# Kernel tuning notes

Measured on AMD Instinct MI355X. Metric: run time of the kernel, lower is better.

The kernel has to match this reference:

```python
import jax, jax.numpy as jnp
import numpy as np

S, B, C, H, W = 2, 100, 5, 224, 224


def setup_inputs() -> dict:
    key = jax.random.key(0)
    ks = jax.random.split(key, 10)
    patches = jax.random.uniform(ks[0], (S, B, C, H, W), jnp.float32)
    translation = jax.random.uniform(ks[1], (S, B, 2), jnp.float32, -0.8, 0.8)
    rotation = jax.random.uniform(ks[2], (S, B), jnp.float32, -np.pi, np.pi)
    scale = jax.random.uniform(ks[3], (S, B), jnp.float32, 0.7, 1.3)
    squeeze = jax.random.uniform(ks[4], (S, B), jnp.float32, 0.8, 1.2)
    shear = jax.random.uniform(ks[5], (S, B), jnp.float32, -0.2, 0.2)
    reds = jax.random.uniform(ks[6], (S, B), jnp.float32, 0.1, 0.5)
    greens = jax.random.uniform(ks[7], (S, B), jnp.float32, 0.1, 0.5)
    blues = jax.random.uniform(ks[8], (S, B), jnp.float32, 0.1, 0.5)
    orders = jax.random.uniform(ks[9], (S, B), jnp.float32)
    return dict(patches=patches, translation=translation, rotation=rotation,
                scale=scale, squeeze=squeeze, shear=shear,
                reds=reds, greens=greens, blues=blues, orders=orders)


def _forward(patches, translation, rotation, scale, squeeze, shear,
             reds, greens, blues, orders):
    s_, b_, c_, h_, w_ = patches.shape
    z = jnp.zeros_like(rotation)
    o = jnp.ones_like(rotation)

    def m3(a11, a12, a13, a21, a22, a23):
        # [S,B,3,3] affine matrix from per-(pop,patch) scalar entries
        r1 = jnp.stack([a11, a12, a13], -1)
        r2 = jnp.stack([a21, a22, a23], -1)
        r3 = jnp.stack([z, z, o], -1)
        return jnp.stack([r1, r2, r3], -2)

    cs, sn = jnp.cos(rotation), jnp.sin(rotation)
    # scale @ rotation @ shear @ translation (same order as the torch module)
    M = (m3(scale * squeeze, z, z, z, scale, z)
         @ m3(cs, -sn, z, sn, cs, z)
         @ m3(o, shear, z, z, o, z)
         @ m3(o, z, translation[..., 0], z, o, translation[..., 1]))
    theta = M[..., :2, :].reshape(s_ * b_, 2, 3)

    # F.affine_grid with align_corners=True: normalized coords in [-1,1]
    xs = jnp.linspace(-1.0, 1.0, w_)[None, :]   # varies along width
    ys = jnp.linspace(-1.0, 1.0, h_)[:, None]   # varies along height
    gx = theta[:, 0, 0, None, None] * xs + theta[:, 0, 1, None, None] * ys + theta[:, 0, 2, None, None]
    gy = theta[:, 1, 0, None, None] * xs + theta[:, 1, 1, None, None] * ys + theta[:, 1, 2, None, None]

    # F.grid_sample bilinear, align_corners=True, zero padding
    ix = (gx + 1.0) * 0.5 * (w_ - 1)
    iy = (gy + 1.0) * 0.5 * (h_ - 1)
    ix0 = jnp.floor(ix)
    iy0 = jnp.floor(iy)
    wx = ix - ix0
    wy = iy - iy0
    ix0i = ix0.astype(jnp.int32)
    iy0i = iy0.astype(jnp.int32)

    P = patches.reshape(s_ * b_, c_, h_, w_)
    gather = jax.vmap(lambda img, y, x: img[:, y, x])  # [C,H,W] per image

    def corner(dy, dx):
        yy = iy0i + dy
        xx = ix0i + dx
        valid = ((yy >= 0) & (yy < h_) & (xx >= 0) & (xx < w_)).astype(patches.dtype)
        v = gather(P, jnp.clip(yy, 0, h_ - 1), jnp.clip(xx, 0, w_ - 1))
        wgt = (wx if dx == 1 else 1.0 - wx) * (wy if dy == 1 else 1.0 - wy) * valid
        return v * wgt[:, None]

    warped = corner(0, 0) + corner(0, 1) + corner(1, 0) + corner(1, 1)
    warped = warped.reshape(s_, b_, c_, h_, w_)

    # RGB colour transform: multiply channels by [r, g, b, 1, order]
    colours = jnp.stack([reds, greens, blues, jnp.ones_like(reds), orders], axis=2)[..., None, None]
    x = warped * colours

    # transparency render: premultiply RGB by alpha, sum over patches, clamp
    rgb = x[:, :, :3] * x[:, :, 3:4]
    y = jnp.clip(rgb.sum(axis=1), 0.0, 1.0)
    return jnp.transpose(y, (0, 2, 3, 1))  # [S,H,W,3]


def reference(patches, translation, rotation, scale, squeeze, shear,
              reds, greens, blues, orders):
    return _forward(patches, translation, rotation, scale, squeeze, shear,
                    reds, greens, blues, orders)
```

## Files before the change

kernel.cpp:

```cpp
#include <hip/hip_runtime.h>

#define SS 2
#define BB 100
#define CC 5
#define HH 224
#define WW 224
#define HW (HH * WW)
#define OUTN (SS * HW * 3)
#define BCHUNK 20
#define NCHUNK (BB / BCHUNK)
#define TILE 16
#define TPD (WW / TILE)
#define TILES_PER_S (TPD * TPD)

__global__ __launch_bounds__(256) void k_reduce(const float* __restrict__ ws,
                                                float* __restrict__ out, int n) {
    int i = blockIdx.x * blockDim.x + threadIdx.x;
    if (i < n) {
        float v = 0.0f;
        #pragma unroll
        for (int c = 0; c < NCHUNK; ++c) v += ws[(size_t)c * OUTN + i];
        out[i] = fminf(fmaxf(v, 0.0f), 1.0f);
    }
}

__global__ __launch_bounds__(256) void k_zero(float* __restrict__ out, int n) {
    int i = blockIdx.x * blockDim.x + threadIdx.x;
    if (i < n) out[i] = 0.0f;
}
__global__ __launch_bounds__(256) void k_clamp(float* __restrict__ out, int n) {
    int i = blockIdx.x * blockDim.x + threadIdx.x;
    if (i < n) { float v = out[i]; out[i] = fminf(fmaxf(v, 0.0f), 1.0f); }
}

template <bool MODE_WS>
__global__ __launch_bounds__(256) void k_main(
    const float* __restrict__ patches,
    const float* __restrict__ tr, const float* __restrict__ rot,
    const float* __restrict__ sc, const float* __restrict__ sq,
    const float* __restrict__ sh, const float* __restrict__ re,
    const float* __restrict__ gr, const float* __restrict__ bl,
    float* __restrict__ dst)
{
    __shared__ float tb[BCHUNK][9];

    const int rem   = blockIdx.x % (SS * TILES_PER_S);
    const int chunk = blockIdx.x / (SS * TILES_PER_S);
    const int s     = rem / TILES_PER_S;
    const int tile  = rem % TILES_PER_S;
    const int tileY = tile / TPD;
    const int tileX = tile % TPD;

    const int tx = threadIdx.x & (TILE - 1);
    const int ty = threadIdx.x >> 4;
    const int w  = tileX * TILE + tx;
    const int h  = tileY * TILE + ty;

    if (threadIdx.x < BCHUNK) {
        const int b = chunk * BCHUNK + threadIdx.x;
        const int i = s * BB + b;
        const float a  = sc[i] * sq[i];
        const float s2 = sc[i];
        float sn, cn;
        sincosf(rot[i], &sn, &cn);
        const float shv = sh[i];
        const float tx_ = tr[2 * i], ty_ = tr[2 * i + 1];
        const float t00 = a * cn;
        const float t01 = a * (cn * shv - sn);
        const float t10 = s2 * sn;
        const float t11 = s2 * (sn * shv + cn);
        tb[threadIdx.x][0] = t00;
        tb[threadIdx.x][1] = t01;
        tb[threadIdx.x][2] = t00 * tx_ + t01 * ty_;
        tb[threadIdx.x][3] = t10;
        tb[threadIdx.x][4] = t11;
        tb[threadIdx.x][5] = t10 * tx_ + t11 * ty_;
        tb[threadIdx.x][6] = re[i];
        tb[threadIdx.x][7] = gr[i];
        tb[threadIdx.x][8] = bl[i];
    }
    __syncthreads();

    const float xs = -1.0f + 2.0f * (float)w / (float)(WW - 1);
    const float ys = -1.0f + 2.0f * (float)h / (float)(HH - 1);

    float accR = 0.0f, accG = 0.0f, accB = 0.0f;

    const float* Pbase = patches + (size_t)s * BB * CC * HW
                                 + (size_t)chunk * BCHUNK * CC * HW;

    for (int bb = 0; bb < BCHUNK; ++bb) {
        const float gx = tb[bb][0] * xs + tb[bb][1] * ys + tb[bb][2];
        const float gy = tb[bb][3] * xs + tb[bb][4] * ys + tb[bb][5];
        const float ix = (gx + 1.0f) * 0.5f * (float)(WW - 1);
        const float iy = (gy + 1.0f) * 0.5f * (float)(HH - 1);

        if (ix <= -1.0f || ix >= (float)WW || iy <= -1.0f || iy >= (float)HH) continue;

        const float ix0f = floorf(ix), iy0f = floorf(iy);
        const float wx = ix - ix0f, wy = iy - iy0f;
        const int ix0 = (int)ix0f, iy0 = (int)iy0f;

        const int x0 = max(ix0, 0);
        const int x1 = min(ix0 + 1, WW - 1);
        const int y0 = max(iy0, 0);
        const int y1 = min(iy0 + 1, HH - 1);

        const float vx0 = (ix0 >= 0)     ? 1.0f : 0.0f;
        const float vx1 = (ix0 + 1 < WW) ? 1.0f : 0.0f;
        const float vy0 = (iy0 >= 0)     ? 1.0f : 0.0f;
        const float vy1 = (iy0 + 1 < HH) ? 1.0f : 0.0f;

        const float w00 = (1.0f - wx) * (1.0f - wy) * vx0 * vy0;
        const float w01 = wx * (1.0f - wy) * vx1 * vy0;
        const float w10 = (1.0f - wx) * wy * vx0 * vy1;
        const float w11 = wx * wy * vx1 * vy1;

        const int i00 = y0 * WW + x0;
        const int i01 = y0 * WW + x1;
        const int i10 = y1 * WW + x0;
        const int i11 = y1 * WW + x1;

        const float* Pb = Pbase + (size_t)bb * CC * HW;

        float chv[4];
        #pragma unroll
        for (int c = 0; c < 4; ++c) {
            const float* Pc = Pb + (size_t)c * HW;
            chv[c] = Pc[i00] * w00 + Pc[i01] * w01 + Pc[i10] * w10 + Pc[i11] * w11;
        }
        const float alpha = chv[3];
        accR += chv[0] * tb[bb][6] * alpha;
        accG += chv[1] * tb[bb][7] * alpha;
        accB += chv[2] * tb[bb][8] * alpha;
    }

    const int pix = s * HW + h * WW + w;
    const size_t o = (size_t)pix * 3;
    if (MODE_WS) {
        float* p = dst + (size_t)chunk * OUTN + o;
        p[0] = accR; p[1] = accG; p[2] = accB;
    } else {
        atomicAdd(&dst[o + 0], accR);
        atomicAdd(&dst[o + 1], accG);
        atomicAdd(&dst[o + 2], accB);
    }
}

extern "C" void kernel_launch(void* const* d_in, const int* in_sizes, int n_in,
                              void* d_out, int out_size, void* d_ws, size_t ws_size,
                              hipStream_t stream) {
    const float* patches = (const float*)d_in[0];
    const float* tr      = (const float*)d_in[1];
    const float* rot     = (const float*)d_in[2];
    const float* sc      = (const float*)d_in[3];
    const float* sq      = (const float*)d_in[4];
    const float* sh      = (const float*)d_in[5];
    const float* re      = (const float*)d_in[6];
    const float* gr      = (const float*)d_in[7];
    const float* bl      = (const float*)d_in[8];
    float* out = (float*)d_out;

    const int nblkOut = (out_size + 255) / 256;
    const int grid    = SS * TILES_PER_S * NCHUNK;

    if (ws_size >= (size_t)NCHUNK * OUTN * sizeof(float)) {
        float* ws = (float*)d_ws;
        k_main<true><<<grid, 256, 0, stream>>>(patches, tr, rot, sc, sq, sh, re, gr, bl, ws);
        k_reduce<<<nblkOut, 256, 0, stream>>>(ws, out, out_size);
    } else {
        k_zero<<<nblkOut, 256, 0, stream>>>(out, out_size);
        k_main<false><<<grid, 256, 0, stream>>>(patches, tr, rot, sc, sq, sh, re, gr, bl, out);
        k_clamp<<<nblkOut, 256, 0, stream>>>(out, out_size);
    }
}
```

Measured before the change: 361.7 us.

## Repack patches into interleaved RGBA float4 layout before bilinear sampling

Adds a pre-pass that transposes the planar RGB+alpha channels of every patch into an interleaved float4 buffer in workspace, so each bilinear corner fetch becomes one 16-byte load instead of four scattered scalar loads. The chunk size per block is halved, doubling the grid and the partial-sum buffer reduced at the end. In exchange it adds a full read and write of about 160 MB of patch data per call, and it only runs if the workspace is large enough.

```diff
diff --git a/kernel.cpp b/kernel.cpp
--- a/kernel.cpp
+++ b/kernel.cpp
@@ -6,12 +6,30 @@
 #define HH 224
 #define WW 224
 #define HW (HH * WW)
+#define IMGN (SS * BB)
 #define OUTN (SS * HW * 3)
-#define BCHUNK 20
+#define BCHUNK 10
 #define NCHUNK (BB / BCHUNK)
 #define TILE 16
 #define TPD (WW / TILE)
 #define TILES_PER_S (TPD * TPD)
+
+#define RGBA_FLOATS ((size_t)IMGN * HW * 4)
+#define PART_FLOATS ((size_t)NCHUNK * OUTN)
+
+__global__ __launch_bounds__(256) void k_repack(const float* __restrict__ patches,
+                                                float4* __restrict__ rgba) {
+    const int i = blockIdx.x * 256 + threadIdx.x;
+    const int img = i / HW;
+    const int hw  = i - img * HW;
+    const float* base = patches + (size_t)img * CC * HW + hw;
+    float4 v;
+    v.x = base[0];
+    v.y = base[HW];
+    v.z = base[2 * HW];
+    v.w = base[3 * HW];
+    rgba[i] = v;
+}
 
 __global__ __launch_bounds__(256) void k_reduce(const float* __restrict__ ws,
                                                 float* __restrict__ out, int n) {
@@ -33,29 +51,9 @@
     if (i < n) { float v = out[i]; out[i] = fminf(fmaxf(v, 0.0f), 1.0f); }
 }
 
-template <bool MODE_WS>
-__global__ __launch_bounds__(256) void k_main(
-    const float* __restrict__ patches,
-    const float* __restrict__ tr, const float* __restrict__ rot,
-    const float* __restrict__ sc, const float* __restrict__ sq,
-    const float* __restrict__ sh, const float* __restrict__ re,
-    const float* __restrict__ gr, const float* __restrict__ bl,
-    float* __restrict__ dst)
-{
-    __shared__ float tb[BCHUNK][9];
-
-    const int rem   = blockIdx.x % (SS * TILES_PER_S);
-    const int chunk = blockIdx.x / (SS * TILES_PER_S);
-    const int s     = rem / TILES_PER_S;
-    const int tile  = rem % TILES_PER_S;
-    const int tileY = tile / TPD;
-    const int tileX = tile % TPD;
-
-    const int tx = threadIdx.x & (TILE - 1);
-    const int ty = threadIdx.x >> 4;
-    const int w  = tileX * TILE + tx;
-    const int h  = tileY * TILE + ty;
-
+__device__ __forceinline__ void setup_tb(float (*tb)[9], int s, int chunk,
+    const float* tr, const float* rot, const float* sc, const float* sq,
+    const float* sh, const float* re, const float* gr, const float* bl) {
     if (threadIdx.x < BCHUNK) {
         const int b = chunk * BCHUNK + threadIdx.x;
         const int i = s * BB + b;
@@ -79,6 +77,112 @@
         tb[threadIdx.x][7] = gr[i];
         tb[threadIdx.x][8] = bl[i];
     }
+}
+
+__global__ __launch_bounds__(256) void k_main_rgba(
+    const float4* __restrict__ rgba,
+    const float* __restrict__ tr, const float* __restrict__ rot,
+    const float* __restrict__ sc, const float* __restrict__ sq,
+    const float* __restrict__ sh, const float* __restrict__ re,
+    const float* __restrict__ gr, const float* __restrict__ bl,
+    float* __restrict__ dst)
+{
+    __shared__ float tb[BCHUNK][9];
+
+    const int rem   = blockIdx.x % (SS * TILES_PER_S);
+    const int chunk = blockIdx.x / (SS * TILES_PER_S);
+    const int s     = rem / TILES_PER_S;
+    const int tile  = rem % TILES_PER_S;
+    const int tileY = tile / TPD;
+    const int tileX = tile % TPD;
+
+    const int tx = threadIdx.x & (TILE - 1);
+    const int ty = threadIdx.x >> 4;
+    const int w  = tileX * TILE + tx;
+    const int h  = tileY * TILE + ty;
+
+    setup_tb(tb, s, chunk, tr, rot, sc, sq, sh, re, gr, bl);
+    __syncthreads();
+
+    const float xs = -1.0f + 2.0f * (float)w / (float)(WW - 1);
+    const float ys = -1.0f + 2.0f * (float)h / (float)(HH - 1);
+
+    float accR = 0.0f, accG = 0.0f, accB = 0.0f;
+
+    const float4* Ibase = rgba + (size_t)(s * BB + chunk * BCHUNK) * HW;
+
+    for (int bb = 0; bb < BCHUNK; ++bb) {
+        const float gx = tb[bb][0] * xs + tb[bb][1] * ys + tb[bb][2];
+        const float gy = tb[bb][3] * xs + tb[bb][4] * ys + tb[bb][5];
+        const float ix = (gx + 1.0f) * 0.5f * (float)(WW - 1);
+        const float iy = (gy + 1.0f) * 0.5f * (float)(HH - 1);
+
+        if (ix <= -1.0f || ix >= (float)WW || iy <= -1.0f || iy >= (float)HH) continue;
+
+        const float ix0f = floorf(ix), iy0f = floorf(iy);
+        const float wx = ix - ix0f, wy = iy - iy0f;
+        const int ix0 = (int)ix0f, iy0 = (int)iy0f;
+
+        const int x0 = max(ix0, 0);
+        const int x1 = min(ix0 + 1, WW - 1);
+        const int y0 = max(iy0, 0);
+        const int y1 = min(iy0 + 1, HH - 1);
+
+        const float vx0 = (ix0 >= 0)     ? 1.0f : 0.0f;
+        const float vx1 = (ix0 + 1 < WW) ? 1.0f : 0.0f;
+        const float vy0 = (iy0 >= 0)     ? 1.0f : 0.0f;
+        const float vy1 = (iy0 + 1 < HH) ? 1.0f : 0.0f;
+
+        const float w00 = (1.0f - wx) * (1.0f - wy) * vx0 * vy0;
+        const float w01 = wx * (1.0f - wy) * vx1 * vy0;
+        const float w10 = (1.0f - wx) * wy * vx0 * vy1;
+        const float w11 = wx * wy * vx1 * vy1;
+
+        const float4* Ib = Ibase + (size_t)bb * HW;
+        const float4 v00 = Ib[y0 * WW + x0];
+        const float4 v01 = Ib[y0 * WW + x1];
+        const float4 v10 = Ib[y1 * WW + x0];
+        const float4 v11 = Ib[y1 * WW + x1];
+
+        const float cr = fmaf(v00.x, w00, fmaf(v01.x, w01, fmaf(v10.x, w10, v11.x * w11)));
+        const float cg = fmaf(v00.y, w00, fmaf(v01.y, w01, fmaf(v10.y, w10, v11.y * w11)));
+        const float cb = fmaf(v00.z, w00, fmaf(v01.z, w01, fmaf(v10.z, w10, v11.z * w11)));
+        const float ca = fmaf(v00.w, w00, fmaf(v01.w, w01, fmaf(v10.w, w10, v11.w * w11)));
+
+        accR = fmaf(cr * tb[bb][6], ca, accR);
+        accG = fmaf(cg * tb[bb][7], ca, accG);
+        accB = fmaf(cb * tb[bb][8], ca, accB);
+    }
+
+    const int pix = s * HW + h * WW + w;
+    float* p = dst + (size_t)chunk * OUTN + (size_t)pix * 3;
+    p[0] = accR; p[1] = accG; p[2] = accB;
+}
+
+template <bool MODE_WS>
+__global__ __launch_bounds__(256) void k_main_planar(
+    const float* __restrict__ patches,
+    const float* __restrict__ tr, const float* __restrict__ rot,
+    const float* __restrict__ sc, const float* __restrict__ sq,
+    const float* __restrict__ sh, const float* __restrict__ re,
+    const float* __restrict__ gr, const float* __restrict__ bl,
+    float* __restrict__ dst)
+{
+    __shared__ float tb[BCHUNK][9];
+
+    const int rem   = blockIdx.x % (SS * TILES_PER_S);
+    const int chunk = blockIdx.x / (SS * TILES_PER_S);
+    const int s     = rem / TILES_PER_S;
+    const int tile  = rem % TILES_PER_S;
+    const int tileY = tile / TPD;
+    const int tileX = tile % TPD;
+
+    const int tx = threadIdx.x & (TILE - 1);
+    const int ty = threadIdx.x >> 4;
+    const int w  = tileX * TILE + tx;
+    const int h  = tileY * TILE + ty;
+
+    setup_tb(tb, s, chunk, tr, rot, sc, sq, sh, re, gr, bl);
     __syncthreads();
 
     const float xs = -1.0f + 2.0f * (float)w / (float)(WW - 1);
@@ -163,14 +267,20 @@
 
     const int nblkOut = (out_size + 255) / 256;
     const int grid    = SS * TILES_PER_S * NCHUNK;
-
-    if (ws_size >= (size_t)NCHUNK * OUTN * sizeof(float)) {
-        float* ws = (float*)d_ws;
-        k_main<true><<<grid, 256, 0, stream>>>(patches, tr, rot, sc, sq, sh, re, gr, bl, ws);
-        k_reduce<<<nblkOut, 256, 0, stream>>>(ws, out, out_size);
+    float* wsf = (float*)d_ws;
+
+    if (ws_size >= (RGBA_FLOATS + PART_FLOATS) * sizeof(float)) {
+        float4* rgba  = (float4*)wsf;
+        float*  parts = wsf + RGBA_FLOATS;
+        k_repack<<<IMGN * HW / 256, 256, 0, stream>>>(patches, rgba);
+        k_main_rgba<<<grid, 256, 0, stream>>>(rgba, tr, rot, sc, sq, sh, re, gr, bl, parts);
+        k_reduce<<<nblkOut, 256, 0, stream>>>(parts, out, out_size);
+    } else if (ws_size >= PART_FLOATS * sizeof(float)) {
+        k_main_planar<true><<<grid, 256, 0, stream>>>(patches, tr, rot, sc, sq, sh, re, gr, bl, wsf);
+        k_reduce<<<nblkOut, 256, 0, stream>>>(wsf, out, out_size);
     } else {
         k_zero<<<nblkOut, 256, 0, stream>>>(out, out_size);
-        k_main<false><<<grid, 256, 0, stream>>>(patches, tr, rot, sc, sq, sh, re, gr, bl, out);
+        k_main_planar<false><<<grid, 256, 0, stream>>>(patches, tr, rot, sc, sq, sh, re, gr, bl, out);
         k_clamp<<<nblkOut, 256, 0, stream>>>(out, out_size);
     }
 }
```

After: 334.2 us. 7.6% less time.
